# Optimization experiments

Measured on AMD Instinct MI355X. Metric: run time of the kernel, lower is better.

Reference implementation:

```python
import math
import jax, jax.numpy as jnp
import numpy as np

AZI = 0.006135923151542565
INC = 0.008267349088394194
EPS = 1e-6
NUM_GROUPS = 32


def group_norm(x, weight, bias, num_groups=NUM_GROUPS, eps=EPS):
    B, C, H, W = x.shape
    xg = x.reshape(B, num_groups, C // num_groups, H, W)
    mean = xg.mean(axis=(2, 3, 4), keepdims=True)
    var = xg.var(axis=(2, 3, 4), keepdims=True)
    xg = (xg - mean) * jax.lax.rsqrt(var + eps)
    x = xg.reshape(B, C, H, W)
    return x * weight[None, :, None, None] + bias[None, :, None, None]


def conv1x1(x, w, b):
    # x: [B,C,H,W], w: [O,C], b: [O]
    return jnp.einsum('bchw,oc->bohw', x, w) + b[None, :, None, None]


def edge_conv(x, r, w1, b1, w2, b2, azi=AZI, inc=INC):
    out = None
    for shift_h in (-1, 0, 1):
        for shift_w in (-1, 0, 1):
            x_s = jnp.roll(x, shift=(shift_w, shift_h), axis=(2, 3))
            r_s = jnp.roll(r, shift=(shift_w, shift_h), axis=(2, 3))
            ca, sa = math.cos(shift_w * azi), math.sin(shift_w * azi)
            ci, si = math.cos(shift_h * inc), math.sin(shift_h * inc)
            pe0 = r_s * (ca * ci) - r
            pe1 = r_s * (ca * si)
            pe2 = r_s * sa
            inp = jnp.concatenate((x_s, x, pe0, pe1, pe2), axis=1)
            h = jax.nn.relu(conv1x1(inp, w1, b1))
            h = conv1x1(h, w2, b2)
            out = h if out is None else jnp.maximum(out, h)
    return out


def setup_inputs() -> dict:
    key = jax.random.key(0)
    ks = jax.random.split(key, 12)
    B, C, W, H = 4, 64, 64, 1024
    O = 64
    Cin1 = 2 * C + 3
    Cin2 = 2 * O + 3

    def lin(k, o, i):
        return jax.random.normal(k, (o, i), dtype=jnp.float32) * (1.0 / np.sqrt(i))

    return {
        'x': jax.random.normal(ks[0], (B, C, W, H), dtype=jnp.float32),
        'r': jax.random.uniform(ks[1], (B, 1, W, H), dtype=jnp.float32),
        'n1_w': jnp.ones((C,), jnp.float32),
        'n1_b': jnp.zeros((C,), jnp.float32),
        'c1_w1': lin(ks[2], O, Cin1),
        'c1_b1': jnp.zeros((O,), jnp.float32),
        'c1_w2': lin(ks[3], O, O),
        'c1_b2': jnp.zeros((O,), jnp.float32),
        'n2_w': jnp.ones((O,), jnp.float32),
        'n2_b': jnp.zeros((O,), jnp.float32),
        'c2_w1': lin(ks[4], O, Cin2),
        'c2_b1': jnp.zeros((O,), jnp.float32),
        'c2_w2': lin(ks[5], O, O),
        'c2_b2': jnp.zeros((O,), jnp.float32),
    }


def reference(x, r, n1_w, n1_b, c1_w1, c1_b1, c1_w2, c1_b2,
              n2_w, n2_b, c2_w1, c2_b1, c2_w2, c2_b2):
    h = group_norm(x, n1_w, n1_b)
    h = jax.nn.relu(h)
    h = edge_conv(h, r, c1_w1, c1_b1, c1_w2, c1_b2)
    h = group_norm(h, n2_w, n2_b)
    h = jax.nn.relu(h)
    # dropout p=0.0 -> identity
    h = edge_conv(h, r, c2_w1, c2_b1, c2_w2, c2_b2)
    return x + h
```

## Files before the change

### kernel.cpp

```cpp
#include <hip/hip_runtime.h>
#include <hip/hip_bf16.h>
#include <cmath>
#include <math.h>

namespace {

constexpr int Bn = 4;
constexpr int Cn = 64;
constexpr int Wn = 64;
constexpr int Hn = 1024;
constexpr int HWn = Wn * Hn;
constexpr int CHWn = Cn * HWn;

typedef float f32x4 __attribute__((ext_vector_type(4)));
typedef short bf16x8 __attribute__((ext_vector_type(8)));
union Frag { uint4 u; bf16x8 s; };

constexpr float kCA[3] = {0.9999811753f, 1.0f, 0.9999811753f};
constexpr float kSA[3] = {-0.0061358846f, 0.0f, 0.0061358846f};
constexpr float kCI[3] = {0.9999658257f, 1.0f, 0.9999658257f};
constexpr float kSI[3] = {-0.0082672549f, 0.0f, 0.0082672549f};

__device__ inline unsigned packbf(float a, float b) {
  union { __hip_bfloat162 h; unsigned u; } c;
  c.h = __float22bfloat162_rn(make_float2(a, b));
  return c.u;
}
__device__ inline float bflo(unsigned d) { return __uint_as_float(d << 16); }
__device__ inline float bfhi(unsigned d) { return __uint_as_float(d & 0xFFFF0000u); }

__global__ __launch_bounds__(256) void gn_partial_kernel(
    const float* __restrict__ x, float* __restrict__ partial) {
  const int bg = blockIdx.x >> 4, part = blockIdx.x & 15;
  const float4* base = (const float4*)(x + (size_t)bg * 2 * HWn) + part * 2048;
  float s = 0.f, s2 = 0.f;
  for (int i = threadIdx.x; i < 2048; i += 256) {
    const float4 v = base[i];
    s += v.x + v.y + v.z + v.w;
    s2 += v.x * v.x + v.y * v.y + v.z * v.z + v.w * v.w;
  }
  #pragma unroll
  for (int off = 32; off > 0; off >>= 1) {
    s  += __shfl_down(s, off, 64);
    s2 += __shfl_down(s2, off, 64);
  }
  __shared__ float red[8];
  const int wid = threadIdx.x >> 6, lid = threadIdx.x & 63;
  if (lid == 0) { red[wid * 2] = s; red[wid * 2 + 1] = s2; }
  __syncthreads();
  if (threadIdx.x == 0) {
    float ts = red[0] + red[2] + red[4] + red[6];
    float t2 = red[1] + red[3] + red[5] + red[7];
    atomicAdd(&partial[bg * 2], ts);
    atomicAdd(&partial[bg * 2 + 1], t2);
  }
}

__global__ void gn_final_kernel(const float* __restrict__ partial,
                                float* __restrict__ stats) {
  const int i = threadIdx.x;
  if (i < 128) {
    const float inv = 1.0f / (2.0f * HWn);
    const float mean = partial[2 * i] * inv;
    const float var = partial[2 * i + 1] * inv - mean * mean;
    stats[2 * i] = mean;
    stats[2 * i + 1] = rsqrtf(var + 1e-6f);
  }
}

__global__ void pack_weights_kernel(const float* __restrict__ w1,
                                    const float* __restrict__ w2,
                                    ushort* __restrict__ w1a, ushort* __restrict__ w1b,
                                    ushort* __restrict__ w2p,
                                    float* __restrict__ vs9, float* __restrict__ pw0) {
  const int t = threadIdx.x;
  for (int i = t; i < 64 * 32; i += 256) {
    const int o = i >> 5, kp = (i & 31) * 2;
    *(unsigned*)&w1a[o * 64 + kp] = packbf(w1[o * 131 + kp], w1[o * 131 + kp + 1]);
    *(unsigned*)&w1b[o * 64 + kp] = packbf(w1[o * 131 + 64 + kp], w1[o * 131 + 64 + kp + 1]);
    *(unsigned*)&w2p[o * 64 + kp] = packbf(w2[o * 64 + kp], w2[o * 64 + kp + 1]);
  }
  if (t < 64) pw0[t] = w1[t * 131 + 128];
  for (int i = t; i < 9 * 64; i += 256) {
    const int s = i >> 6, k = i & 63;
    const int isw = s / 3, ish = s % 3;
    const float m0 = kCA[isw] * kCI[ish];
    const float m1 = kCA[isw] * kSI[ish];
    const float m2 = kSA[isw];
    vs9[s * 64 + k] = m0 * w1[k * 131 + 128] + m1 * w1[k * 131 + 129] +
                      m2 * w1[k * 131 + 130];
  }
}

__global__ __launch_bounds__(256, 2) void dual_gemm_kernel(
    const float* __restrict__ x, const float* __restrict__ stats,
    const float* __restrict__ gw, const float* __restrict__ gb,
    const ushort* __restrict__ w1a, const ushort* __restrict__ w1b,
    const float* __restrict__ b1,
    ushort* __restrict__ Y, ushort* __restrict__ Z) {
  __shared__ float2 scsh[64];
  __shared__ float bias[64];
  __shared__ __align__(16) ushort dsY[64 * 72];
  __shared__ __align__(16) ushort dsZ[64 * 72];
  const int blk = blockIdx.x;
  const int h0 = (blk & 15) * 64;
  const int w  = (blk >> 4) & 63;
  const int b  = blk >> 10;
  const int t  = threadIdx.x;
  const int lane = t & 63, wv = t >> 6;
  const int n = lane & 15, q = lane >> 4;

  if (t < 64) {
    const int g = t >> 1;
    const float mean = stats[(b * 32 + g) * 2];
    const float rstd = stats[(b * 32 + g) * 2 + 1];
    const float sc = rstd * gw[t];
    scsh[t] = make_float2(sc, gb[t] - mean * sc);
    bias[t] = b1[t];
  }
  __syncthreads();

  const int jg = h0 + wv * 16 + n;
  const float* xb = x + (size_t)b * CHWn + (size_t)w * Hn;
  Frag Bf[2];
  #pragma unroll
  for (int kh = 0; kh < 2; kh++) {
    unsigned d[4];
    #pragma unroll
    for (int p = 0; p < 4; p++) {
      const int c0 = kh * 32 + q * 8 + p * 2;
      const float2 s0 = scsh[c0], s1 = scsh[c0 + 1];
      const float v0 = fmaxf(xb[(size_t)c0 * HWn + jg] * s0.x + s0.y, 0.f);
      const float v1 = fmaxf(xb[(size_t)(c0 + 1) * HWn + jg] * s1.x + s1.y, 0.f);
      d[p] = packbf(v0, v1);
    }
    Bf[kh].u = make_uint4(d[0], d[1], d[2], d[3]);
  }

  f32x4 accY[4], accZ[4];
  #pragma unroll
  for (int os = 0; os < 4; os++) { accY[os] = (f32x4)0.f; accZ[os] = (f32x4)0.f; }

  #pragma unroll
  for (int os = 0; os < 4; os++) {
    const int o = os * 16 + n;
    #pragma unroll
    for (int kh = 0; kh < 2; kh++) {
      const int k = kh * 32 + q * 8;
      Frag fa, fb;
      fa.u = *(const uint4*)&w1a[o * 64 + k];
      fb.u = *(const uint4*)&w1b[o * 64 + k];
      accY[os] = __builtin_amdgcn_mfma_f32_16x16x32_bf16(fa.s, Bf[kh].s, accY[os], 0, 0, 0);
      accZ[os] = __builtin_amdgcn_mfma_f32_16x16x32_bf16(fb.s, Bf[kh].s, accZ[os], 0, 0, 0);
    }
  }

  const int jl = wv * 16 + n;
  #pragma unroll
  for (int os = 0; os < 4; os++) {
    #pragma unroll
    for (int rp = 0; rp < 4; rp += 2) {
      const int o = os * 16 + q * 4 + rp;
      *(unsigned*)&dsY[jl * 72 + o] = packbf(accY[os][rp], accY[os][rp + 1]);
      *(unsigned*)&dsZ[jl * 72 + o] =
          packbf(accZ[os][rp] + bias[o], accZ[os][rp + 1] + bias[o + 1]);
    }
  }
  __syncthreads();

  #pragma unroll
  for (int p = 0; p < 2; p++) {
    const int slot = t + 256 * p;
    const int j = slot >> 3, og = slot & 7;
    const size_t gidx = (((size_t)b * Wn + w) * Hn + h0 + j) * 64 + og * 8;
    *(uint4*)&Y[gidx] = *(const uint4*)&dsY[j * 72 + og * 8];
    *(uint4*)&Z[gidx] = *(const uint4*)&dsZ[j * 72 + og * 8];
  }
}

__global__ __launch_bounds__(256, 3) void shift_max_kernel(
    const ushort* __restrict__ Y, const ushort* __restrict__ Z,
    const float* __restrict__ r, const float* __restrict__ vs9,
    const float* __restrict__ pw0, const ushort* __restrict__ w2p,
    const float* __restrict__ b2,
    const float* __restrict__ xres, const int add_res,
    float* __restrict__ out) {
  __shared__ __align__(16) ushort ys[2][66 * 72];
  __shared__ float rsh[3][68];
  __shared__ __align__(16) float vsl[9 * 64];
  const int blk = blockIdx.x;
  const int h0 = (blk & 15) * 64;
  const int w  = (blk >> 4) & 63;
  const int b  = blk >> 10;
  const int t  = threadIdx.x;
  const int lane = t & 63, wv = t >> 6;
  const int n = lane & 15, q = lane >> 4;
  const int jl = wv * 16 + n;

  if (t < 144) ((float4*)vsl)[t] = ((const float4*)vs9)[t];
  for (int i = t; i < 3 * 66; i += 256) {
    const int wi = i / 66, jj = i - wi * 66;
    const int wsrc = (w + wi - 1 + 64) & 63;
    const int hsrc = (h0 + jj - 1 + 1024) & 1023;
    rsh[wi][jj] = r[(size_t)b * HWn + wsrc * Hn + hsrc];
  }
  {
    const int wsrc = (w + 1) & 63;
    #pragma unroll
    for (int p = 0; p < 3; p++) {
      const int slot = t + 256 * p;
      if (slot < 66 * 8) {
        const int jj = slot >> 3, kg = slot & 7;
        const int hsrc = (h0 + jj - 1 + 1024) & 1023;
        *(uint4*)&ys[0][jj * 72 + kg * 8] =
            *(const uint4*)&Y[(((size_t)b * Wn + wsrc) * Hn + hsrc) * 64 + kg * 8];
      }
    }
  }

  Frag A[8];
  #pragma unroll
  for (int os = 0; os < 4; os++) {
    const int o = os * 16 + n;
    #pragma unroll
    for (int kh = 0; kh < 2; kh++)
      A[os * 2 + kh].u = *(const uint4*)&w2p[o * 64 + kh * 32 + q * 8];
  }

  const float rc = r[(size_t)b * HWn + (size_t)w * Hn + h0 + jl];
  float zcA[8], zcB[8];
  {
    const size_t zbase = (((size_t)b * Wn + w) * Hn + h0 + jl) * 64;
    const uint4 z0 = *(const uint4*)&Z[zbase + q * 8];
    const uint4 z1 = *(const uint4*)&Z[zbase + 32 + q * 8];
    const float4 pwA0 = *(const float4*)&pw0[q * 8];
    const float4 pwA1 = *(const float4*)&pw0[q * 8 + 4];
    const float4 pwB0 = *(const float4*)&pw0[32 + q * 8];
    const float4 pwB1 = *(const float4*)&pw0[32 + q * 8 + 4];
    const float pwA[8] = {pwA0.x, pwA0.y, pwA0.z, pwA0.w, pwA1.x, pwA1.y, pwA1.z, pwA1.w};
    const float pwB[8] = {pwB0.x, pwB0.y, pwB0.z, pwB0.w, pwB1.x, pwB1.y, pwB1.z, pwB1.w};
    const unsigned zw0[4] = {z0.x, z0.y, z0.z, z0.w};
    const unsigned zw1[4] = {z1.x, z1.y, z1.z, z1.w};
    #pragma unroll
    for (int p = 0; p < 4; p++) {
      zcA[2 * p]     = bflo(zw0[p]) - rc * pwA[2 * p];
      zcA[2 * p + 1] = bfhi(zw0[p]) - rc * pwA[2 * p + 1];
      zcB[2 * p]     = bflo(zw1[p]) - rc * pwB[2 * p];
      zcB[2 * p + 1] = bfhi(zw1[p]) - rc * pwB[2 * p + 1];
    }
  }

  __syncthreads();

  f32x4 om[4];
  #pragma unroll
  for (int os = 0; os < 4; os++) om[os] = (f32x4)(-INFINITY);

  int cur = 0;
  for (int sw = -1; sw <= 1; sw++) {
    const int isw = sw + 1;
    uint4 g0, g1, g2;
    if (sw < 1) {
      const int wsrc = (w - (sw + 1) + 64) & 63;
      const size_t ybase = ((size_t)b * Wn + wsrc) * Hn;
      {
        const int jj = t >> 3, kg = t & 7;
        const int hsrc = (h0 + jj - 1 + 1024) & 1023;
        g0 = *(const uint4*)&Y[(ybase + hsrc) * 64 + kg * 8];
      }
      {
        const int slot = t + 256;
        const int jj = slot >> 3, kg = slot & 7;
        const int hsrc = (h0 + jj - 1 + 1024) & 1023;
        g1 = *(const uint4*)&Y[(ybase + hsrc) * 64 + kg * 8];
      }
      if (t + 512 < 66 * 8) {
        const int slot = t + 512;
        const int jj = slot >> 3, kg = slot & 7;
        const int hsrc = (h0 + jj - 1 + 1024) & 1023;
        g2 = *(const uint4*)&Y[(ybase + hsrc) * 64 + kg * 8];
      }
    }

    #pragma unroll
    for (int sh = -1; sh <= 1; sh++) {
      const int ish = sh + 1;
      const float rsv = rsh[1 - sw][jl - sh + 1];
      const float* vrow = &vsl[(isw * 3 + ish) * 64];
      const float4 vA0 = *(const float4*)&vrow[q * 8];
      const float4 vA1 = *(const float4*)&vrow[q * 8 + 4];
      const float4 vB0 = *(const float4*)&vrow[32 + q * 8];
      const float4 vB1 = *(const float4*)&vrow[32 + q * 8 + 4];
      const float vsA[8] = {vA0.x, vA0.y, vA0.z, vA0.w, vA1.x, vA1.y, vA1.z, vA1.w};
      const float vsB[8] = {vB0.x, vB0.y, vB0.z, vB0.w, vB1.x, vB1.y, vB1.z, vB1.w};
      const int yrow = (jl - sh + 1) * 72;
      const uint4 y0 = *(const uint4*)&ys[cur][yrow + q * 8];
      const uint4 y1 = *(const uint4*)&ys[cur][yrow + 32 + q * 8];
      const unsigned yw0[4] = {y0.x, y0.y, y0.z, y0.w};
      const unsigned yw1[4] = {y1.x, y1.y, y1.z, y1.w};
      unsigned hw0[4], hw1[4];
      #pragma unroll
      for (int p = 0; p < 4; p++) {
        const float hA0 = fmaf(rsv, vsA[2 * p],     bflo(yw0[p]) + zcA[2 * p]);
        const float hA1 = fmaf(rsv, vsA[2 * p + 1], bfhi(yw0[p]) + zcA[2 * p + 1]);
        hw0[p] = packbf(fmaxf(hA0, 0.f), fmaxf(hA1, 0.f));
        const float hB0 = fmaf(rsv, vsB[2 * p],     bflo(yw1[p]) + zcB[2 * p]);
        const float hB1 = fmaf(rsv, vsB[2 * p + 1], bfhi(yw1[p]) + zcB[2 * p + 1]);
        hw1[p] = packbf(fmaxf(hB0, 0.f), fmaxf(hB1, 0.f));
      }
      Frag Bf0, Bf1;
      Bf0.u = make_uint4(hw0[0], hw0[1], hw0[2], hw0[3]);
      Bf1.u = make_uint4(hw1[0], hw1[1], hw1[2], hw1[3]);
      #pragma unroll
      for (int os = 0; os < 4; os++) {
        f32x4 acc = (f32x4)0.f;
        acc = __builtin_amdgcn_mfma_f32_16x16x32_bf16(A[os * 2].s, Bf0.s, acc, 0, 0, 0);
        acc = __builtin_amdgcn_mfma_f32_16x16x32_bf16(A[os * 2 + 1].s, Bf1.s, acc, 0, 0, 0);
        #pragma unroll
        for (int e = 0; e < 4; e++) om[os][e] = fmaxf(om[os][e], acc[e]);
      }
    }

    if (sw < 1) {
      {
        const int jj = t >> 3, kg = t & 7;
        *(uint4*)&ys[cur ^ 1][jj * 72 + kg * 8] = g0;
      }
      {
        const int slot = t + 256;
        const int jj = slot >> 3, kg = slot & 7;
        *(uint4*)&ys[cur ^ 1][jj * 72 + kg * 8] = g1;
      }
      if (t + 512 < 66 * 8) {
        const int slot = t + 512;
        const int jj = slot >> 3, kg = slot & 7;
        *(uint4*)&ys[cur ^ 1][jj * 72 + kg * 8] = g2;
      }
    }
    __syncthreads();
    cur ^= 1;
  }

  const int jgl = h0 + jl;
  #pragma unroll
  for (int os = 0; os < 4; os++) {
    #pragma unroll
    for (int e = 0; e < 4; e++) {
      const int o = os * 16 + q * 4 + e;
      const size_t idx = ((size_t)b * Cn + o) * HWn + (size_t)w * Hn + jgl;
      float v = om[os][e] + b2[o];
      if (add_res) v += xres[idx];
      out[idx] = v;
    }
  }
}

}

extern "C" void kernel_launch(void* const* d_in, const int* in_sizes, int n_in,
                              void* d_out, int out_size, void* d_ws, size_t ws_size,
                              hipStream_t stream) {
  const float* x    = (const float*)d_in[0];
  const float* r    = (const float*)d_in[1];
  const float* n1w  = (const float*)d_in[2];
  const float* n1b  = (const float*)d_in[3];
  const float* c1w1 = (const float*)d_in[4];
  const float* c1b1 = (const float*)d_in[5];
  const float* c1w2 = (const float*)d_in[6];
  const float* c1b2 = (const float*)d_in[7];
  const float* n2w  = (const float*)d_in[8];
  const float* n2b  = (const float*)d_in[9];
  const float* c2w1 = (const float*)d_in[10];
  const float* c2b1 = (const float*)d_in[11];
  const float* c2w2 = (const float*)d_in[12];
  const float* c2b2 = (const float*)d_in[13];
  float* out = (float*)d_out;

  float* partial = (float*)d_ws;
  float* statsf  = partial + 256;
  float* vs9     = partial + 512;
  float* pw0     = partial + 1088;
  ushort* Ybf = (ushort*)((char*)d_ws + 8192);
  ushort* Zbf = Ybf + (size_t)Bn * Wn * Hn * 64;
  ushort* w1a = Zbf + (size_t)Bn * Wn * Hn * 64;
  ushort* w1b = w1a + 64 * 64;
  ushort* w2p = w1b + 64 * 64;

  hipMemsetAsync(partial, 0, 256 * sizeof(float), stream);
  gn_partial_kernel<<<2048, 256, 0, stream>>>(x, partial);
  gn_final_kernel<<<1, 128, 0, stream>>>(partial, statsf);
  pack_weights_kernel<<<1, 256, 0, stream>>>(c1w1, c1w2, w1a, w1b, w2p, vs9, pw0);
  dual_gemm_kernel<<<4096, 256, 0, stream>>>(x, statsf, n1w, n1b, w1a, w1b, c1b1, Ybf, Zbf);
  shift_max_kernel<<<4096, 256, 0, stream>>>(Ybf, Zbf, r, vs9, pw0, w2p, c1b2, x, 0, out);
  hipMemsetAsync(partial, 0, 256 * sizeof(float), stream);
  gn_partial_kernel<<<2048, 256, 0, stream>>>(out, partial);
  gn_final_kernel<<<1, 128, 0, stream>>>(partial, statsf);
  pack_weights_kernel<<<1, 256, 0, stream>>>(c2w1, c2w2, w1a, w1b, w2p, vs9, pw0);
  dual_gemm_kernel<<<4096, 256, 0, stream>>>(out, statsf, n2w, n2b, w1a, w1b, c2b1, Ybf, Zbf);
  shift_max_kernel<<<4096, 256, 0, stream>>>(Ybf, Zbf, r, vs9, pw0, w2p, c2b2, x, 1, out);
}
```

Before: 437.5 us.

## Stage Y tiles into LDS via direct global_load_lds with XOR swizzle

Replaces the register-staged global loads and LDS stores for the shifted Y columns with direct global-to-LDS 16-byte loads. The LDS row padding becomes an XOR swizzle on the 16-byte chunk index so bank conflicts stay low, and occupancy is pinned to 4 waves per EU. The aim is to cut register pressure and VGPR round-trips during the prefetch and let it overlap the MFMA work. It relies on the hardware writing lane-contiguous LDS addresses and on correct waitcnt handling before the barrier, and the final trailing barrier is dropped.

```diff
diff --git a/kernel.cpp b/kernel.cpp
--- a/kernel.cpp
+++ b/kernel.cpp
@@ -28,6 +28,12 @@
 }
 __device__ inline float bflo(unsigned d) { return __uint_as_float(d << 16); }
 __device__ inline float bfhi(unsigned d) { return __uint_as_float(d & 0xFFFF0000u); }
+
+__device__ inline void gload16(const void* g, void* l) {
+  __builtin_amdgcn_global_load_lds(
+      (const __attribute__((address_space(1))) void*)g,
+      (__attribute__((address_space(3))) void*)l, 16, 0, 0);
+}
 
 __global__ __launch_bounds__(256) void gn_partial_kernel(
     const float* __restrict__ x, float* __restrict__ partial) {
@@ -178,14 +184,16 @@
   }
 }
 
-__global__ __launch_bounds__(256, 3) void shift_max_kernel(
+__global__ __launch_bounds__(256)
+__attribute__((amdgpu_waves_per_eu(4, 4)))
+void shift_max_kernel(
     const ushort* __restrict__ Y, const ushort* __restrict__ Z,
     const float* __restrict__ r, const float* __restrict__ vs9,
     const float* __restrict__ pw0, const ushort* __restrict__ w2p,
     const float* __restrict__ b2,
     const float* __restrict__ xres, const int add_res,
     float* __restrict__ out) {
-  __shared__ __align__(16) ushort ys[2][66 * 72];
+  __shared__ __align__(16) ushort ys[2][66 * 64];
   __shared__ float rsh[3][68];
   __shared__ __align__(16) float vsl[9 * 64];
   const int blk = blockIdx.x;
@@ -197,25 +205,31 @@
   const int n = lane & 15, q = lane >> 4;
   const int jl = wv * 16 + n;
 
+  const ushort* Yb = Y + (size_t)b * (size_t)Wn * Hn * 64;
+
+  auto stage_col = [&](int bufidx, int wsrc) {
+    const size_t ybase = (size_t)wsrc * (Hn * 64);
+    #pragma unroll
+    for (int p = 0; p < 3; p++) {
+      const int slot = t + 256 * p;
+      if (slot < 66 * 8) {
+        const int jj = slot >> 3, S = slot & 7;
+        const int G = S ^ (jj & 7);
+        const int hsrc = (h0 + jj - 1 + 1024) & 1023;
+        gload16(&Yb[ybase + (size_t)hsrc * 64 + G * 8],
+                &ys[bufidx][(wv * 64 + 256 * p) * 8]);
+      }
+    }
+  };
+
+  stage_col(0, (w + 1) & 63);
+
   if (t < 144) ((float4*)vsl)[t] = ((const float4*)vs9)[t];
   for (int i = t; i < 3 * 66; i += 256) {
     const int wi = i / 66, jj = i - wi * 66;
     const int wsrc = (w + wi - 1 + 64) & 63;
     const int hsrc = (h0 + jj - 1 + 1024) & 1023;
     rsh[wi][jj] = r[(size_t)b * HWn + wsrc * Hn + hsrc];
-  }
-  {
-    const int wsrc = (w + 1) & 63;
-    #pragma unroll
-    for (int p = 0; p < 3; p++) {
-      const int slot = t + 256 * p;
-      if (slot < 66 * 8) {
-        const int jj = slot >> 3, kg = slot & 7;
-        const int hsrc = (h0 + jj - 1 + 1024) & 1023;
-        *(uint4*)&ys[0][jj * 72 + kg * 8] =
-            *(const uint4*)&Y[(((size_t)b * Wn + wsrc) * Hn + hsrc) * 64 + kg * 8];
-      }
-    }
   }
 
   Frag A[8];
@@ -259,28 +273,7 @@
   int cur = 0;
   for (int sw = -1; sw <= 1; sw++) {
     const int isw = sw + 1;
-    uint4 g0, g1, g2;
-    if (sw < 1) {
-      const int wsrc = (w - (sw + 1) + 64) & 63;
-      const size_t ybase = ((size_t)b * Wn + wsrc) * Hn;
-      {
-        const int jj = t >> 3, kg = t & 7;
-        const int hsrc = (h0 + jj - 1 + 1024) & 1023;
-        g0 = *(const uint4*)&Y[(ybase + hsrc) * 64 + kg * 8];
-      }
-      {
-        const int slot = t + 256;
-        const int jj = slot >> 3, kg = slot & 7;
-        const int hsrc = (h0 + jj - 1 + 1024) & 1023;
-        g1 = *(const uint4*)&Y[(ybase + hsrc) * 64 + kg * 8];
-      }
-      if (t + 512 < 66 * 8) {
-        const int slot = t + 512;
-        const int jj = slot >> 3, kg = slot & 7;
-        const int hsrc = (h0 + jj - 1 + 1024) & 1023;
-        g2 = *(const uint4*)&Y[(ybase + hsrc) * 64 + kg * 8];
-      }
-    }
+    if (sw < 1) stage_col(cur ^ 1, (w - (sw + 1) + 64) & 63);
 
     #pragma unroll
     for (int sh = -1; sh <= 1; sh++) {
@@ -293,9 +286,11 @@
       const float4 vB1 = *(const float4*)&vrow[32 + q * 8 + 4];
       const float vsA[8] = {vA0.x, vA0.y, vA0.z, vA0.w, vA1.x, vA1.y, vA1.z, vA1.w};
       const float vsB[8] = {vB0.x, vB0.y, vB0.z, vB0.w, vB1.x, vB1.y, vB1.z, vB1.w};
-      const int yrow = (jl - sh + 1) * 72;
-      const uint4 y0 = *(const uint4*)&ys[cur][yrow + q * 8];
-      const uint4 y1 = *(const uint4*)&ys[cur][yrow + 32 + q * 8];
+      const int ro = jl - sh + 1;
+      const int sA = (q ^ (ro & 7)) * 8;
+      const int sB = ((q + 4) ^ (ro & 7)) * 8;
+      const uint4 y0 = *(const uint4*)&ys[cur][ro * 64 + sA];
+      const uint4 y1 = *(const uint4*)&ys[cur][ro * 64 + sB];
       const unsigned yw0[4] = {y0.x, y0.y, y0.z, y0.w};
       const unsigned yw1[4] = {y1.x, y1.y, y1.z, y1.w};
       unsigned hw0[4], hw1[4];
@@ -322,23 +317,9 @@
     }
 
     if (sw < 1) {
-      {
-        const int jj = t >> 3, kg = t & 7;
-        *(uint4*)&ys[cur ^ 1][jj * 72 + kg * 8] = g0;
-      }
-      {
-        const int slot = t + 256;
-        const int jj = slot >> 3, kg = slot & 7;
-        *(uint4*)&ys[cur ^ 1][jj * 72 + kg * 8] = g1;
-      }
-      if (t + 512 < 66 * 8) {
-        const int slot = t + 512;
-        const int jj = slot >> 3, kg = slot & 7;
-        *(uint4*)&ys[cur ^ 1][jj * 72 + kg * 8] = g2;
-      }
-    }
-    __syncthreads();
-    cur ^= 1;
+      __syncthreads();
+      cur ^= 1;
+    }
   }
 
   const int jgl = h0 + jl;
```

Measured after the change: 520.9 us. 1.19x slower.
